# Kernel tuning notes

Hardware: AMD Instinct MI355X
Metric: run time of the kernel (lower is better)

The kernel has to match this reference:

```python
import jax, jax.numpy as jnp
import numpy as np

N = 50000   # nodes
E = 800000  # edges
D = 128     # input_size == hidden_size
R = 4       # n_relations
L = 3       # n_layers


def setup_inputs() -> dict:
    key = jax.random.key(0)
    ks = jax.random.split(key, 8)
    x = jax.random.normal(ks[0], (N, D), dtype=jnp.float32)
    edge_index = jax.random.randint(ks[1], (2, E), 0, N, dtype=jnp.int32)
    edge_type = jax.random.randint(ks[2], (E,), 0, R, dtype=jnp.int32)
    scale = 1.0 / np.sqrt(D)
    W = jax.random.normal(ks[3], (L, R, D, D), dtype=jnp.float32) * scale      # per-relation weights
    root = jax.random.normal(ks[4], (L, D, D), dtype=jnp.float32) * scale      # root (self) weights
    bias = jnp.zeros((L, D), dtype=jnp.float32)
    gamma = jnp.ones((L, D), dtype=jnp.float32)   # LayerNorm weight
    beta = jnp.zeros((L, D), dtype=jnp.float32)   # LayerNorm bias
    return {"x": x, "edge_index": edge_index, "edge_type": edge_type,
            "W": W, "root": root, "bias": bias, "gamma": gamma, "beta": beta}


def _rgcn_conv(x, src, dst, etype, W_r, W_root, b):
    # Transform all nodes by every relation weight once: [R, N, D]
    h = jnp.einsum('ni,rio->rno', x, W_r)
    msg = h[etype, src]                                   # [E, D] per-edge messages
    # mean aggregation per (dst, relation), matching PyG RGCNConv aggr='mean'
    seg = dst * R + etype                                 # combined segment id
    cnt = jax.ops.segment_sum(jnp.ones((E,), x.dtype), seg, num_segments=N * R)
    inv = 1.0 / jnp.maximum(cnt, 1.0)
    agg = jax.ops.segment_sum(msg * inv[seg][:, None], dst, num_segments=N)
    return agg + x @ W_root + b


def _layernorm(x, g, b, eps=1e-5):
    mu = jnp.mean(x, axis=-1, keepdims=True)
    var = jnp.var(x, axis=-1, keepdims=True)
    return (x - mu) * jax.lax.rsqrt(var + eps) * g + b


def reference(x, edge_index, edge_type, W, root, bias, gamma, beta):
    src, dst = edge_index[0], edge_index[1]
    for i in range(L):
        x_res = x
        x = _rgcn_conv(x, src, dst, edge_type, W[i], root[i], bias[i])
        x = jax.nn.relu(x)
        # dropout p=0.0 -> no-op; residual_projection is Identity (input_size==hidden_size)
        x = x + x_res
        x = _layernorm(x, gamma[i], beta[i])
    return x
```

## Files before the change

### kernel.cpp

```cpp
#include <hip/hip_runtime.h>
#include <stdint.h>

#define NN 50000
#define EE 800000
#define DD 128
#define RR 4
#define LL 3
#define NRSEG (NN*RR)
#define NKB 20
#define NBK 196
#define BKCAP 5120
#define WCONV_T (LL*NKB*8*64)

typedef _Float16 f16;
typedef _Float16 f16x8 __attribute__((ext_vector_type(8)));
typedef float f32x4 __attribute__((ext_vector_type(4)));

union U32H { uint32_t u; f16 h[2]; };
union U4H  { uint4 u; f16 h[8]; };

__global__ __launch_bounds__(1024) void k_binA(const int* __restrict__ ei, const int* __restrict__ et,
                                               int* __restrict__ bcur, int2* __restrict__ tmp){
  __shared__ int bcnt[256];
  __shared__ int lbase[256];
  __shared__ int gbase[256];
  __shared__ int s[256];
  __shared__ int tot;
  __shared__ int2 stage[4096];
  int t = threadIdx.x;
  if(t < 256) bcnt[t] = 0;
  __syncthreads();

  int seg[4], src[4], bk[4], rk[4];
  #pragma unroll
  for(int j=0;j<4;j++){
    int e = blockIdx.x*4096 + j*1024 + t;
    if(e < EE){
      src[j] = ei[e];
      seg[j] = ei[EE+e]*RR + et[e];
      bk[j]  = seg[j] >> 10;
      rk[j]  = atomicAdd(&bcnt[bk[j]], 1);
    } else { seg[j] = -1; }
  }
  __syncthreads();

  if(t < 256) s[t] = bcnt[t];
  __syncthreads();
  for(int o=1;o<256;o<<=1){
    int x = (t<256 && t>=o) ? s[t-o] : 0;
    __syncthreads();
    if(t<256) s[t] += x;
    __syncthreads();
  }
  if(t < 256){
    lbase[t] = s[t] - bcnt[t];
    if(t == 255) tot = s[255];
    if(t < NBK && bcnt[t] > 0) gbase[t] = atomicAdd(&bcur[t], bcnt[t]);
  }
  __syncthreads();

  #pragma unroll
  for(int j=0;j<4;j++){
    if(seg[j] >= 0){
      int2 p; p.x = seg[j]; p.y = src[j];
      stage[lbase[bk[j]] + rk[j]] = p;
    }
  }
  __syncthreads();

  int T = tot;
  #pragma unroll
  for(int j=0;j<4;j++){
    int idx = j*1024 + t;
    if(idx < T){
      int2 p = stage[idx];
      int bb = p.x >> 10;
      tmp[(size_t)bb*BKCAP + gbase[bb] + (idx - lbase[bb])] = p;
    }
  }
}

__global__ __launch_bounds__(256) void k_prefix(const int* __restrict__ bcur, int* __restrict__ boff){
  __shared__ int s[256];
  int t = threadIdx.x;
  int v = (t < NBK) ? bcur[t] : 0;
  s[t] = v; __syncthreads();
  for(int o=1;o<256;o<<=1){ int x=(t>=o)?s[t-o]:0; __syncthreads(); s[t]+=x; __syncthreads(); }
  if(t < NBK) boff[t] = s[t] - v;
}

__global__ __launch_bounds__(1024) void k_binB(const int* __restrict__ boff, const int* __restrict__ bcur,
                                               const int2* __restrict__ tmp,
                                               int* __restrict__ rowp, int* __restrict__ ssrc){
  __shared__ int hist[1024];
  __shared__ int sc[1024];
  __shared__ int cur[1024];
  int b = blockIdx.x, t = threadIdx.x;
  hist[t] = 0;
  __syncthreads();
  int n = bcur[b];
  const int2* src = tmp + (size_t)b*BKCAP;
  for(int i = t; i < n; i += 1024) atomicAdd(&hist[src[i].x & 1023], 1);
  __syncthreads();
  sc[t] = hist[t]; __syncthreads();
  for(int o=1;o<1024;o<<=1){ int x=(t>=o)?sc[t-o]:0; __syncthreads(); sc[t]+=x; __syncthreads(); }
  int gb = boff[b];
  int excl = gb + sc[t] - hist[t];
  cur[t] = excl;
  int idx = b*1024 + t;
  if(idx < NRSEG) rowp[idx] = excl;
  if(b == NBK-1 && t == 0) rowp[NRSEG] = gb + sc[1023];
  __syncthreads();
  for(int i = t; i < n; i += 1024){
    int2 p = src[i];
    int pos = atomicAdd(&cur[p.x & 1023], 1);
    ssrc[pos] = p.y;
  }
}

__global__ __launch_bounds__(256) void k_convWX(const float* __restrict__ W, const float* __restrict__ root,
                                                f16* __restrict__ Wf,
                                                const float* __restrict__ x, f16* __restrict__ x16){
  int t = blockIdx.x*256 + threadIdx.x;
  if(t < WCONV_T){
    int lane = t & 63;
    int cb   = (t>>6) & 7;
    int kb   = (t>>9) % NKB;
    int l    = (t>>9) / NKB;
    int col  = cb*16 + (lane&15);
    int kbase= kb*32 + (lane>>4)*8;
    f16* dst = Wf + (size_t)t*8;
    #pragma unroll
    for(int e=0;e<8;e++){
      int k = kbase+e;
      float v = (k < 4*DD) ? W[(((size_t)l*RR + (k>>7))*DD + (k&127))*DD + col]
                           : root[((size_t)l*DD + (k-4*DD))*DD + col];
      dst[e] = (f16)v;
    }
  } else {
    int u = t - WCONV_T;
    if(u < NN*DD/8){
      const float4* xf = (const float4*)x + (size_t)u*2;
      float4 a = xf[0], b = xf[1];
      U4H o;
      o.h[0]=(f16)a.x; o.h[1]=(f16)a.y; o.h[2]=(f16)a.z; o.h[3]=(f16)a.w;
      o.h[4]=(f16)b.x; o.h[5]=(f16)b.y; o.h[6]=(f16)b.z; o.h[7]=(f16)b.w;
      ((uint4*)x16)[u] = o.u;
    }
  }
}

__device__ __forceinline__ void acc8(float a[8], uint4 v){
  U4H w; w.u = v;
  #pragma unroll
  for(int k=0;k<8;k++) a[k] += (float)w.h[k];
}

__global__ __launch_bounds__(256) void k_agg(const f16* __restrict__ x16, const int* __restrict__ rowp,
                                             const int* __restrict__ ssrc, f16* __restrict__ A16){
  int seg = blockIdx.x*16 + (threadIdx.x >> 4);
  int l   = threadIdx.x & 15;
  if(seg >= NRSEG) return;

  int b = rowp[seg], e = rowp[seg+1];
  int n = e - b;
  const uint4* xl = (const uint4*)x16 + l;

  float acc[8];
  #pragma unroll
  for(int k=0;k<8;k++) acc[k] = 0.f;

  for(int base=0; base<n; base+=4){
    int m = n - base;
    int i0 = b + base;
    int c0 = ssrc[i0];
    int c1 = (m>1) ? ssrc[i0+1] : c0;
    int c2 = (m>2) ? ssrc[i0+2] : c0;
    int c3 = (m>3) ? ssrc[i0+3] : c0;
    uint4 v0 = xl[(size_t)c0*16];
    uint4 v1 = xl[(size_t)c1*16];
    uint4 v2 = xl[(size_t)c2*16];
    uint4 v3 = xl[(size_t)c3*16];
    acc8(acc, v0);
    if(m>1) acc8(acc, v1);
    if(m>2) acc8(acc, v2);
    if(m>3) acc8(acc, v3);
  }

  float inv = 1.f/(float)max(n,1);
  U4H o;
  #pragma unroll
  for(int k=0;k<8;k++) o.h[k] = (f16)(acc[k]*inv);
  ((uint4*)A16)[(size_t)seg*16 + l] = o.u;
}

__device__ __forceinline__ void stageB(const f16* __restrict__ Wf, f16* lds, int kb, int wid, int lane){
  const f16* src = Wf + (size_t)kb*4096;
  #pragma unroll
  for(int j=wid;j<8;j+=4){
    __builtin_amdgcn_global_load_lds((const __attribute__((address_space(1))) void*)(src + j*512 + lane*8),
                                     (__attribute__((address_space(3))) void*)(lds + j*512), 16, 0, 0);
  }
}

template<int LAST>
__global__ __launch_bounds__(256) void k_gemm(const f16* __restrict__ A16, const f16* __restrict__ x16,
                                              const f16* __restrict__ Wf,
                                              const float* __restrict__ bias, const float* __restrict__ gmm,
                                              const float* __restrict__ bet,
                                              f16* __restrict__ xnext, float* __restrict__ outf){
  __shared__ f16 Blds[2][4096];
  int tid  = threadIdx.x;
  int lane = tid & 63, wid = tid >> 6;
  int rbase = blockIdx.x*128 + wid*32;
  int fr = lane & 15, kg = lane >> 4;

  int arow0 = rbase + fr;       if(arow0 >= NN) arow0 = NN-1;
  int arow1 = rbase + 16 + fr;  if(arow1 >= NN) arow1 = NN-1;
  const f16* Ar0 = A16 + (size_t)arow0*512 + kg*8;
  const f16* Ar1 = A16 + (size_t)arow1*512 + kg*8;
  const f16* Xr0 = x16 + (size_t)arow0*128 + kg*8;
  const f16* Xr1 = x16 + (size_t)arow1*128 + kg*8;

  f32x4 acc[2][8];
  #pragma unroll
  for(int r=0;r<2;r++)
    #pragma unroll
    for(int c=0;c<8;c++) acc[r][c] = (f32x4){0.f,0.f,0.f,0.f};

  f16x8 a0, a1;
  a0 = *(const f16x8*)(Ar0); a1 = *(const f16x8*)(Ar1);
  stageB(Wf, &Blds[0][0], 0, wid, lane);

  for(int kb=0; kb<NKB; kb++){
    __syncthreads();
    if(kb+1 < NKB) stageB(Wf, &Blds[(kb+1)&1][0], kb+1, wid, lane);
    f16x8 na0 = a0, na1 = a1;
    if(kb+1 < NKB){
      if(kb+1 < 16){ na0 = *(const f16x8*)(Ar0 + (kb+1)*32); na1 = *(const f16x8*)(Ar1 + (kb+1)*32); }
      else         { na0 = *(const f16x8*)(Xr0 + (kb+1-16)*32); na1 = *(const f16x8*)(Xr1 + (kb+1-16)*32); }
    }
    const f16* bb = &Blds[kb&1][lane*8];
    #pragma unroll
    for(int cb=0;cb<8;cb++){
      f16x8 b = *(const f16x8*)(bb + cb*512);
      acc[0][cb] = __builtin_amdgcn_mfma_f32_16x16x32_f16(a0, b, acc[0][cb], 0, 0, 0);
      acc[1][cb] = __builtin_amdgcn_mfma_f32_16x16x32_f16(a1, b, acc[1][cb], 0, 0, 0);
    }
    a0 = na0; a1 = na1;
  }

  float bs[8];
  #pragma unroll
  for(int cb=0;cb<8;cb++) bs[cb] = bias[cb*16 + fr];
  int g4 = kg*4;
  #pragma unroll
  for(int rh=0; rh<2; rh++){
    float vv[8][4];
    #pragma unroll
    for(int cb=0;cb<8;cb++){
      int col = cb*16 + fr;
      #pragma unroll
      for(int q=0;q<4;q++){
        float v = acc[rh][cb][q] + bs[cb];
        v = v > 0.f ? v : 0.f;
        int row = rbase + rh*16 + g4 + q;
        float res = (row < NN) ? (float)x16[(size_t)row*128 + col] : 0.f;
        vv[cb][q] = v + res;
      }
    }
    #pragma unroll
    for(int q=0;q<4;q++){
      float s1=0.f, s2=0.f;
      #pragma unroll
      for(int cb=0;cb<8;cb++){ float v=vv[cb][q]; s1+=v; s2+=v*v; }
      #pragma unroll
      for(int m=1;m<16;m<<=1){ s1 += __shfl_xor(s1,m,16); s2 += __shfl_xor(s2,m,16); }
      float mu  = s1*(1.f/128.f);
      float var = s2*(1.f/128.f) - mu*mu;
      float rs  = rsqrtf(var + 1e-5f);
      int row = rbase + rh*16 + g4 + q;
      if(row < NN){
        #pragma unroll
        for(int cb=0;cb<8;cb++){
          int col = cb*16 + fr;
          float y = (vv[cb][q]-mu)*rs*gmm[col] + bet[col];
          if(LAST) outf[(size_t)row*128 + col] = y;
          else     xnext[(size_t)row*128 + col] = (f16)y;
        }
      }
    }
  }
}

extern "C" void kernel_launch(void* const* d_in, const int* in_sizes, int n_in,
                              void* d_out, int out_size, void* d_ws, size_t ws_size,
                              hipStream_t stream){
  const float* x    = (const float*)d_in[0];
  const int*   ei   = (const int*)d_in[1];
  const int*   et   = (const int*)d_in[2];
  const float* W    = (const float*)d_in[3];
  const float* root = (const float*)d_in[4];
  const float* bias = (const float*)d_in[5];
  const float* gmm  = (const float*)d_in[6];
  const float* bet  = (const float*)d_in[7];

  char* ws = (char*)d_ws;
  int*   bcur = (int*)(ws + 0);
  int*   boff = (int*)(ws + 1024);
  int*   rowp = (int*)(ws + 2048);
  int*   ssrc = (int*)(ws + 804096);
  f16*   Wf   = (f16*)(ws + 4004096);
  f16*   x16a = (f16*)(ws + 4495616);
  f16*   x16b = (f16*)(ws + 17295616);
  f16*   A16  = (f16*)(ws + 30095616);
  int2*  tmp  = (int2*)A16;

  hipMemsetAsync(bcur, 0, 784, stream);
  k_binA  <<<NBK, 1024, 0, stream>>>(ei, et, bcur, tmp);
  k_prefix<<<1, 256, 0, stream>>>(bcur, boff);
  k_binB  <<<NBK, 1024, 0, stream>>>(boff, bcur, tmp, rowp, ssrc);
  k_convWX<<<(WCONV_T + NN*DD/8 + 255)/256, 256, 0, stream>>>(W, root, Wf, x, x16a);

  f16* xc = x16a; f16* xn = x16b;
  for(int l=0; l<LL; l++){
    k_agg<<<NRSEG/16, 256, 0, stream>>>(xc, rowp, ssrc, A16);
    if(l < LL-1)
      k_gemm<0><<<(NN+127)/128, 256, 0, stream>>>(A16, xc, Wf + (size_t)l*81920,
                                                  bias+l*DD, gmm+l*DD, bet+l*DD, xn, nullptr);
    else
      k_gemm<1><<<(NN+127)/128, 256, 0, stream>>>(A16, xc, Wf + (size_t)l*81920,
                                                  bias+l*DD, gmm+l*DD, bet+l*DD, nullptr, (float*)d_out);
    f16* t = xc; xc = xn; xn = t;
  }
}
```

Baseline: 228.0 us.

## Fuse mean aggregation into GEMM via LDS tile and fold prefix into binB

The per-(dst,relation) mean aggregation now runs inside the GEMM kernel. Each 512-thread block gathers 64 nodes × 4 relations into a swizzled LDS A-tile, so the fp16 A16 intermediate is never written to or reread from global memory. The separate k_prefix launch is removed, and each k_binB block computes its own bucket offset by reducing the earlier bucket counts. The trade-offs are a large 64 KB LDS tile that limits occupancy, LayerNorm now reducing across two waves through shared memory, and the gather and MFMA phases running serially within each block.

```diff
diff --git a/kernel.cpp b/kernel.cpp
--- a/kernel.cpp
+++ b/kernel.cpp
@@ -16,7 +16,6 @@
 typedef _Float16 f16x8 __attribute__((ext_vector_type(8)));
 typedef float f32x4 __attribute__((ext_vector_type(4)));
 
-union U32H { uint32_t u; f16 h[2]; };
 union U4H  { uint4 u; f16 h[8]; };
 
 __global__ __launch_bounds__(1024) void k_binA(const int* __restrict__ ei, const int* __restrict__ et,
@@ -80,36 +79,36 @@
   }
 }
 
-__global__ __launch_bounds__(256) void k_prefix(const int* __restrict__ bcur, int* __restrict__ boff){
-  __shared__ int s[256];
-  int t = threadIdx.x;
-  int v = (t < NBK) ? bcur[t] : 0;
-  s[t] = v; __syncthreads();
-  for(int o=1;o<256;o<<=1){ int x=(t>=o)?s[t-o]:0; __syncthreads(); s[t]+=x; __syncthreads(); }
-  if(t < NBK) boff[t] = s[t] - v;
-}
-
-__global__ __launch_bounds__(1024) void k_binB(const int* __restrict__ boff, const int* __restrict__ bcur,
-                                               const int2* __restrict__ tmp,
+__global__ __launch_bounds__(1024) void k_binB(const int* __restrict__ bcur, const int2* __restrict__ tmp,
                                                int* __restrict__ rowp, int* __restrict__ ssrc){
   __shared__ int hist[1024];
   __shared__ int sc[1024];
   __shared__ int cur[1024];
+  __shared__ int pre[256];
   int b = blockIdx.x, t = threadIdx.x;
   hist[t] = 0;
-  __syncthreads();
+  if(t < 256) pre[t] = (t < b) ? bcur[t] : 0;
+  __syncthreads();
+  for(int o=128;o>0;o>>=1){ if(t<o) pre[t]+=pre[t+o]; __syncthreads(); }
+  int gb = pre[0];
+  __syncthreads();
+  if(b == NBK-1){
+    if(t < 256) pre[t] = (t < NBK) ? bcur[t] : 0;
+    __syncthreads();
+    for(int o=128;o>0;o>>=1){ if(t<o) pre[t]+=pre[t+o]; __syncthreads(); }
+    if(t==0) rowp[NRSEG] = pre[0];
+    __syncthreads();
+  }
   int n = bcur[b];
   const int2* src = tmp + (size_t)b*BKCAP;
   for(int i = t; i < n; i += 1024) atomicAdd(&hist[src[i].x & 1023], 1);
   __syncthreads();
   sc[t] = hist[t]; __syncthreads();
   for(int o=1;o<1024;o<<=1){ int x=(t>=o)?sc[t-o]:0; __syncthreads(); sc[t]+=x; __syncthreads(); }
-  int gb = boff[b];
   int excl = gb + sc[t] - hist[t];
   cur[t] = excl;
   int idx = b*1024 + t;
   if(idx < NRSEG) rowp[idx] = excl;
-  if(b == NBK-1 && t == 0) rowp[NRSEG] = gb + sc[1023];
   __syncthreads();
   for(int i = t; i < n; i += 1024){
     int2 p = src[i];
@@ -156,138 +155,138 @@
   for(int k=0;k<8;k++) a[k] += (float)w.h[k];
 }
 
-__global__ __launch_bounds__(256) void k_agg(const f16* __restrict__ x16, const int* __restrict__ rowp,
-                                             const int* __restrict__ ssrc, f16* __restrict__ A16){
-  int seg = blockIdx.x*16 + (threadIdx.x >> 4);
-  int l   = threadIdx.x & 15;
-  if(seg >= NRSEG) return;
-
-  int b = rowp[seg], e = rowp[seg+1];
-  int n = e - b;
-  const uint4* xl = (const uint4*)x16 + l;
-
-  float acc[8];
-  #pragma unroll
-  for(int k=0;k<8;k++) acc[k] = 0.f;
-
-  for(int base=0; base<n; base+=4){
-    int m = n - base;
-    int i0 = b + base;
-    int c0 = ssrc[i0];
-    int c1 = (m>1) ? ssrc[i0+1] : c0;
-    int c2 = (m>2) ? ssrc[i0+2] : c0;
-    int c3 = (m>3) ? ssrc[i0+3] : c0;
-    uint4 v0 = xl[(size_t)c0*16];
-    uint4 v1 = xl[(size_t)c1*16];
-    uint4 v2 = xl[(size_t)c2*16];
-    uint4 v3 = xl[(size_t)c3*16];
-    acc8(acc, v0);
-    if(m>1) acc8(acc, v1);
-    if(m>2) acc8(acc, v2);
-    if(m>3) acc8(acc, v3);
-  }
-
-  float inv = 1.f/(float)max(n,1);
-  U4H o;
-  #pragma unroll
-  for(int k=0;k<8;k++) o.h[k] = (f16)(acc[k]*inv);
-  ((uint4*)A16)[(size_t)seg*16 + l] = o.u;
-}
-
-__device__ __forceinline__ void stageB(const f16* __restrict__ Wf, f16* lds, int kb, int wid, int lane){
-  const f16* src = Wf + (size_t)kb*4096;
-  #pragma unroll
-  for(int j=wid;j<8;j+=4){
-    __builtin_amdgcn_global_load_lds((const __attribute__((address_space(1))) void*)(src + j*512 + lane*8),
-                                     (__attribute__((address_space(3))) void*)(lds + j*512), 16, 0, 0);
-  }
-}
-
 template<int LAST>
-__global__ __launch_bounds__(256) void k_gemm(const f16* __restrict__ A16, const f16* __restrict__ x16,
-                                              const f16* __restrict__ Wf,
-                                              const float* __restrict__ bias, const float* __restrict__ gmm,
-                                              const float* __restrict__ bet,
-                                              f16* __restrict__ xnext, float* __restrict__ outf){
+__global__ __launch_bounds__(512, 4) void k_fused(const f16* __restrict__ x16, const int* __restrict__ rowp,
+                                                  const int* __restrict__ ssrc, const f16* __restrict__ Wf,
+                                                  const float* __restrict__ bias, const float* __restrict__ gmm,
+                                                  const float* __restrict__ bet,
+                                                  f16* __restrict__ xnext, float* __restrict__ outf){
+  __shared__ f16 At[64*512];
   __shared__ f16 Blds[2][4096];
   int tid  = threadIdx.x;
   int lane = tid & 63, wid = tid >> 6;
-  int rbase = blockIdx.x*128 + wid*32;
+  int blk  = blockIdx.x;
+  int rbase = blk*64;
+
+  __builtin_amdgcn_global_load_lds(
+      (const __attribute__((address_space(1))) void*)(Wf + wid*512 + lane*8),
+      (__attribute__((address_space(3))) void*)(&Blds[0][wid*512]), 16, 0, 0);
+
+  {
+    int g = tid >> 4, l = tid & 15;
+    const uint4* xl = (const uint4*)x16 + l;
+    #pragma unroll 1
+    for(int si=0; si<8; ++si){
+      int seg_local = g*8 + si;
+      int gseg = blk*256 + seg_local;
+      int b=0, n=0;
+      if(gseg < NRSEG){ b = rowp[gseg]; n = rowp[gseg+1] - b; }
+      float acc[8];
+      #pragma unroll
+      for(int k=0;k<8;k++) acc[k]=0.f;
+      for(int base=0; base<n; base+=4){
+        int m = n - base;
+        int i0 = b + base;
+        int c0 = ssrc[i0];
+        int c1 = (m>1) ? ssrc[i0+1] : c0;
+        int c2 = (m>2) ? ssrc[i0+2] : c0;
+        int c3 = (m>3) ? ssrc[i0+3] : c0;
+        uint4 v0 = xl[(size_t)c0*16];
+        uint4 v1 = xl[(size_t)c1*16];
+        uint4 v2 = xl[(size_t)c2*16];
+        uint4 v3 = xl[(size_t)c3*16];
+        acc8(acc, v0);
+        if(m>1) acc8(acc, v1);
+        if(m>2) acc8(acc, v2);
+        if(m>3) acc8(acc, v3);
+      }
+      float inv = 1.f/(float)max(n,1);
+      U4H o;
+      #pragma unroll
+      for(int k=0;k<8;k++) o.h[k] = (f16)(acc[k]*inv);
+      int row = seg_local >> 2;
+      int col_h = (seg_local&3)*128 + l*8;
+      *(uint4*)&At[row*512 + (col_h ^ ((row&7)<<3))] = o.u;
+    }
+  }
+
   int fr = lane & 15, kg = lane >> 4;
-
-  int arow0 = rbase + fr;       if(arow0 >= NN) arow0 = NN-1;
-  int arow1 = rbase + 16 + fr;  if(arow1 >= NN) arow1 = NN-1;
-  const f16* Ar0 = A16 + (size_t)arow0*512 + kg*8;
-  const f16* Ar1 = A16 + (size_t)arow1*512 + kg*8;
-  const f16* Xr0 = x16 + (size_t)arow0*128 + kg*8;
-  const f16* Xr1 = x16 + (size_t)arow1*128 + kg*8;
-
-  f32x4 acc[2][8];
-  #pragma unroll
-  for(int r=0;r<2;r++)
-    #pragma unroll
-    for(int c=0;c<8;c++) acc[r][c] = (f32x4){0.f,0.f,0.f,0.f};
-
-  f16x8 a0, a1;
-  a0 = *(const f16x8*)(Ar0); a1 = *(const f16x8*)(Ar1);
-  stageB(Wf, &Blds[0][0], 0, wid, lane);
+  int wr = wid >> 1, wc = wid & 1;
+  int arow = rbase + wr*16 + fr; if(arow >= NN) arow = NN-1;
+  const f16* Xr = x16 + (size_t)arow*128 + kg*8;
+  int rowA = wr*16 + fr;
+  int abase = rowA*512, axor = (rowA&7)<<3;
+
+  f32x4 acc[4];
+  #pragma unroll
+  for(int c=0;c<4;c++) acc[c] = (f32x4){0.f,0.f,0.f,0.f};
 
   for(int kb=0; kb<NKB; kb++){
     __syncthreads();
-    if(kb+1 < NKB) stageB(Wf, &Blds[(kb+1)&1][0], kb+1, wid, lane);
-    f16x8 na0 = a0, na1 = a1;
-    if(kb+1 < NKB){
-      if(kb+1 < 16){ na0 = *(const f16x8*)(Ar0 + (kb+1)*32); na1 = *(const f16x8*)(Ar1 + (kb+1)*32); }
-      else         { na0 = *(const f16x8*)(Xr0 + (kb+1-16)*32); na1 = *(const f16x8*)(Xr1 + (kb+1-16)*32); }
-    }
-    const f16* bb = &Blds[kb&1][lane*8];
-    #pragma unroll
-    for(int cb=0;cb<8;cb++){
-      f16x8 b = *(const f16x8*)(bb + cb*512);
-      acc[0][cb] = __builtin_amdgcn_mfma_f32_16x16x32_f16(a0, b, acc[0][cb], 0, 0, 0);
-      acc[1][cb] = __builtin_amdgcn_mfma_f32_16x16x32_f16(a1, b, acc[1][cb], 0, 0, 0);
-    }
-    a0 = na0; a1 = na1;
-  }
-
-  float bs[8];
-  #pragma unroll
-  for(int cb=0;cb<8;cb++) bs[cb] = bias[cb*16 + fr];
+    if(kb+1 < NKB)
+      __builtin_amdgcn_global_load_lds(
+          (const __attribute__((address_space(1))) void*)(Wf + (size_t)(kb+1)*4096 + wid*512 + lane*8),
+          (__attribute__((address_space(3))) void*)(&Blds[(kb+1)&1][wid*512]), 16, 0, 0);
+    f16x8 a;
+    if(kb < 16) a = *(const f16x8*)&At[abase + ((kb*32 + kg*8) ^ axor)];
+    else        a = *(const f16x8*)(Xr + (kb-16)*32);
+    const f16* bb = &Blds[kb&1][(wc*4)*512 + lane*8];
+    #pragma unroll
+    for(int cbl=0;cbl<4;cbl++){
+      f16x8 b = *(const f16x8*)(bb + cbl*512);
+      acc[cbl] = __builtin_amdgcn_mfma_f32_16x16x32_f16(a, b, acc[cbl], 0, 0, 0);
+    }
+  }
+
+  float* sred = (float*)At;
+  float bs[4];
+  #pragma unroll
+  for(int c=0;c<4;c++) bs[c] = bias[wc*64 + c*16 + fr];
   int g4 = kg*4;
-  #pragma unroll
-  for(int rh=0; rh<2; rh++){
-    float vv[8][4];
-    #pragma unroll
-    for(int cb=0;cb<8;cb++){
-      int col = cb*16 + fr;
+  float vv[4][4];
+  #pragma unroll
+  for(int cbl=0;cbl<4;cbl++){
+    int col = wc*64 + cbl*16 + fr;
+    #pragma unroll
+    for(int q=0;q<4;q++){
+      float v = acc[cbl][q] + bs[cbl];
+      v = v > 0.f ? v : 0.f;
+      int row = rbase + wr*16 + g4 + q;
+      float res = (row < NN) ? (float)x16[(size_t)row*128 + col] : 0.f;
+      vv[cbl][q] = v + res;
+    }
+  }
+  __syncthreads();
+  #pragma unroll
+  for(int q=0;q<4;q++){
+    float s1=0.f, s2=0.f;
+    #pragma unroll
+    for(int cbl=0;cbl<4;cbl++){ float v=vv[cbl][q]; s1+=v; s2+=v*v; }
+    #pragma unroll
+    for(int m=1;m<16;m<<=1){ s1 += __shfl_xor(s1,m,16); s2 += __shfl_xor(s2,m,16); }
+    if(fr == 0){
+      int rin = wr*16 + g4 + q;
+      sred[(0*2+wc)*64 + rin] = s1;
+      sred[(1*2+wc)*64 + rin] = s2;
+    }
+  }
+  __syncthreads();
+  #pragma unroll
+  for(int q=0;q<4;q++){
+    int rin = wr*16 + g4 + q;
+    float S1 = sred[0*128 + rin] + sred[0*128 + 64 + rin];
+    float S2 = sred[1*128 + rin] + sred[1*128 + 64 + rin];
+    float mu  = S1*(1.f/128.f);
+    float var = S2*(1.f/128.f) - mu*mu;
+    float rs  = rsqrtf(var + 1e-5f);
+    int row = rbase + wr*16 + g4 + q;
+    if(row < NN){
       #pragma unroll
-      for(int q=0;q<4;q++){
-        float v = acc[rh][cb][q] + bs[cb];
-        v = v > 0.f ? v : 0.f;
-        int row = rbase + rh*16 + g4 + q;
-        float res = (row < NN) ? (float)x16[(size_t)row*128 + col] : 0.f;
-        vv[cb][q] = v + res;
-      }
-    }
-    #pragma unroll
-    for(int q=0;q<4;q++){
-      float s1=0.f, s2=0.f;
-      #pragma unroll
-      for(int cb=0;cb<8;cb++){ float v=vv[cb][q]; s1+=v; s2+=v*v; }
-      #pragma unroll
-      for(int m=1;m<16;m<<=1){ s1 += __shfl_xor(s1,m,16); s2 += __shfl_xor(s2,m,16); }
-      float mu  = s1*(1.f/128.f);
-      float var = s2*(1.f/128.f) - mu*mu;
-      float rs  = rsqrtf(var + 1e-5f);
-      int row = rbase + rh*16 + g4 + q;
-      if(row < NN){
-        #pragma unroll
-        for(int cb=0;cb<8;cb++){
-          int col = cb*16 + fr;
-          float y = (vv[cb][q]-mu)*rs*gmm[col] + bet[col];
-          if(LAST) outf[(size_t)row*128 + col] = y;
-          else     xnext[(size_t)row*128 + col] = (f16)y;
-        }
+      for(int cbl=0;cbl<4;cbl++){
+        int col = wc*64 + cbl*16 + fr;
+        float y = (vv[cbl][q]-mu)*rs*gmm[col] + bet[col];
+        if(LAST) outf[(size_t)row*128 + col] = y;
+        else     xnext[(size_t)row*128 + col] = (f16)y;
       }
     }
   }
@@ -307,30 +306,26 @@
 
   char* ws = (char*)d_ws;
   int*   bcur = (int*)(ws + 0);
-  int*   boff = (int*)(ws + 1024);
   int*   rowp = (int*)(ws + 2048);
   int*   ssrc = (int*)(ws + 804096);
   f16*   Wf   = (f16*)(ws + 4004096);
   f16*   x16a = (f16*)(ws + 4495616);
   f16*   x16b = (f16*)(ws + 17295616);
-  f16*   A16  = (f16*)(ws + 30095616);
-  int2*  tmp  = (int2*)A16;
+  int2*  tmp  = (int2*)(ws + 30095616);
 
   hipMemsetAsync(bcur, 0, 784, stream);
   k_binA  <<<NBK, 1024, 0, stream>>>(ei, et, bcur, tmp);
-  k_prefix<<<1, 256, 0, stream>>>(bcur, boff);
-  k_binB  <<<NBK, 1024, 0, stream>>>(boff, bcur, tmp, rowp, ssrc);
+  k_binB  <<<NBK, 1024, 0, stream>>>(bcur, tmp, rowp, ssrc);
   k_convWX<<<(WCONV_T + NN*DD/8 + 255)/256, 256, 0, stream>>>(W, root, Wf, x, x16a);
 
   f16* xc = x16a; f16* xn = x16b;
   for(int l=0; l<LL; l++){
-    k_agg<<<NRSEG/16, 256, 0, stream>>>(xc, rowp, ssrc, A16);
     if(l < LL-1)
-      k_gemm<0><<<(NN+127)/128, 256, 0, stream>>>(A16, xc, Wf + (size_t)l*81920,
-                                                  bias+l*DD, gmm+l*DD, bet+l*DD, xn, nullptr);
+      k_fused<0><<<(NN+63)/64, 512, 0, stream>>>(xc, rowp, ssrc, Wf + (size_t)l*81920,
+                                                 bias+l*DD, gmm+l*DD, bet+l*DD, xn, nullptr);
     else
-      k_gemm<1><<<(NN+127)/128, 256, 0, stream>>>(A16, xc, Wf + (size_t)l*81920,
-                                                  bias+l*DD, gmm+l*DD, bet+l*DD, nullptr, (float*)d_out);
+      k_fused<1><<<(NN+63)/64, 512, 0, stream>>>(xc, rowp, ssrc, Wf + (size_t)l*81920,
+                                                 bias+l*DD, gmm+l*DD, bet+l*DD, nullptr, (float*)d_out);
     f16* t = xc; xc = xn; xn = t;
   }
 }
```

Measured after the change: 264.5 us. 1.16x slower.
